# Optimization experiments

Measured on AMD Instinct MI355X. Metric: run time of the kernel, lower is better.

Reference implementation:

```python
import jax, jax.numpy as jnp
import numpy as np

# dims: M scalars (0e), K vectors (1e) in input; T = tp_features; N = batch of atoms
M, K, T, N = 128, 64, 64, 131072
D_IN = M + 3 * K  # 320, e3nn layout: [128x0e | 64x1e flattened as (mul, 3)]


def _act_norm(f):
    # e3nn Activation normalizes act so E_{z~N(0,1)}[act(z)^2] = 1
    z = np.linspace(-8.0, 8.0, 20001)
    pdf = np.exp(-0.5 * z * z) / np.sqrt(2.0 * np.pi)
    return float(np.sqrt(np.trapz(f(z) ** 2 * pdf, z)))

C_SILU = _act_norm(lambda z: z / (1.0 + np.exp(-z)))
C_RELU = _act_norm(lambda z: np.maximum(z, 0.0))
INV_SQRT_M = float(1.0 / np.sqrt(M))
INV_SQRT_K = float(1.0 / np.sqrt(K))
INV_SQRT_3 = float(1.0 / np.sqrt(3.0))  # wigner_3j(1,1,0) = delta_ij/sqrt(3)
TP_NORM = float(1.0 / np.sqrt(2.0 * T * T))  # fan-in over the 2 paths into 0e


def setup_inputs() -> dict:
    key = jax.random.key(0)
    ks = jax.random.split(key, 11)
    f32 = jnp.float32
    return {
        "x": jax.random.normal(ks[0], (N, D_IN), f32),
        "input_shift": jnp.zeros((D_IN,), f32),
        "output_scale": jnp.ones((), f32),
        # PerceptronLayer 1: Linear (Mx0e+Kx1e) -> ((M+K)x0e + Kx1e)
        "w0_1": jax.random.normal(ks[1], (M, M + K), f32),
        "b0_1": jnp.zeros((M + K,), f32),
        "w1_1": jax.random.normal(ks[2], (K, K), f32),
        # PerceptronLayer 2 (same irreps, resnet applies)
        "w0_2": jax.random.normal(ks[3], (M, M + K), f32),
        "b0_2": jnp.zeros((M + K,), f32),
        "w1_2": jax.random.normal(ks[4], (K, K), f32),
        # linear_out: (Mx0e+Kx1e) -> (Tx0e+Tx1e)
        "w0_o": jax.random.normal(ks[5], (M, T), f32),
        "b0_o": jnp.zeros((T,), f32),
        "w1_o": jax.random.normal(ks[6], (K, T), f32),
        # FullyConnectedTensorProduct (tp, tp) -> 1x0e: paths 0e*0e->0e, 1e*1e->0e
        "w_tp0": jax.random.normal(ks[7], (T, T), f32),
        "w_tp1": jax.random.normal(ks[8], (T, T), f32),
    }


def _linear(xs, xv, w0, b0, w1):
    # e3nn o3.Linear: per-irrep dense mixing with 1/sqrt(fan_in), bias on 0e only
    ys = xs @ w0 * INV_SQRT_M + b0          # [N, M+K] scalars + gates
    yv = jnp.einsum('nki,kj->nji', xv, w1) * INV_SQRT_K  # [N, K, 3]
    return ys, yv


def _gate(ys, yv):
    # e3nn Gate: silu on 0e scalars, relu on 0e gates, gate the 1e vectors
    s = jax.nn.silu(ys[:, :M]) / C_SILU     # [N, M]
    g = jax.nn.relu(ys[:, M:]) / C_RELU     # [N, K]
    return s, yv * g[:, :, None]


def reference(x, input_shift, output_scale,
              w0_1, b0_1, w1_1, w0_2, b0_2, w1_2,
              w0_o, b0_o, w1_o, w_tp0, w_tp1):
    x = x - input_shift
    xs = x[:, :M]                           # [N, M] 0e block
    xv = x[:, M:].reshape(-1, K, 3)         # [N, K, 3] 1e block
    for (w0, b0, w1) in ((w0_1, b0_1, w1_1), (w0_2, b0_2, w1_2)):
        ys, yv = _linear(xs, xv, w0, b0, w1)
        s, v = _gate(ys, yv)
        xs = xs + s                         # resnet: irreps_in == irreps_out
        xv = xv + v
    # linear_out -> irreps_tp = Tx0e + Tx1e
    zs = xs @ w0_o * INV_SQRT_M + b0_o                    # [N, T]
    zv = jnp.einsum('nki,kj->nji', xv, w1_o) * INV_SQRT_K # [N, T, 3]
    # FullyConnectedTensorProduct(z, z) -> 0e (avoid [N,T,T] blowup)
    y0 = jnp.sum((zs @ w_tp0) * zs, axis=-1)                                    # [N]
    y1 = jnp.sum(jnp.einsum('nui,uv->nvi', zv, w_tp1) * zv, axis=(1, 2)) * INV_SQRT_3
    y = (y0 + y1) * TP_NORM / output_scale
    return y[:, None]
```

## Files before the change

kernel.cpp:

```cpp
#include <hip/hip_runtime.h>
#include <math.h>


typedef _Float16 f16;
typedef _Float16 f16x8 __attribute__((ext_vector_type(8)));
typedef __fp16   fp16x2 __attribute__((ext_vector_type(2)));
typedef float    f32x4 __attribute__((ext_vector_type(4)));
typedef int      i32x4 __attribute__((ext_vector_type(4)));

#define MFMA16(a, b, c) __builtin_amdgcn_mfma_f32_16x16x32_f16(a, b, c, 0, 0, 0)

constexpr float INV_SQRT_M = 0.08838834764831845f;
constexpr float INV_SQRT_K = 0.125f;
constexpr float INV_SQRT_3 = 0.57735026918962576f;
constexpr float TP_NORM    = 0.011048543456039806f;

#define OFF_W01 0
#define OFF_W11 24576
#define OFF_W02 28672
#define OFF_W12 53248
#define OFF_W0O 57344
#define OFF_W1O 65536
#define OFF_TP0 69632
#define OFF_TP1 73728
#define PACK_UNITS 9728
#define FB01 38912
#define FB02 39104
#define FB0O 39296
#define TOTAL_UNITS (PACK_UNITS + 448)

#define LDS_W1     24576
#define LDS_BIAS_F 14336
#define LDS_W0O    0
#define LDS_W1O    8192
#define LDS_TP0    12288
#define LDS_TP1    16384
#define LDS_B0O_F  10240

#define NTHR 512

__global__ void pack_and_consts(const float* __restrict__ w01, const float* __restrict__ w11,
                                const float* __restrict__ w02, const float* __restrict__ w12,
                                const float* __restrict__ w0o, const float* __restrict__ w1o,
                                const float* __restrict__ tp0, const float* __restrict__ tp1,
                                const float* __restrict__ b01, const float* __restrict__ b02,
                                const float* __restrict__ b0o,
                                f16* __restrict__ dst, float* __restrict__ ws) {
    if (blockIdx.x == 40) {
        __shared__ double red[256];
        const int t = threadIdx.x;
        double acc_s = 0.0, acc_r = 0.0;
        for (int i = t; i <= 20000; i += 256) {
            const double z = -8.0 + (16.0 * (double)i) / 20000.0;
            const double pdf = exp(-0.5 * z * z) / 2.5066282746310002;
            const double sil = z / (1.0 + exp(-z));
            const double wgt = (i == 0 || i == 20000) ? 0.5 : 1.0;
            acc_s += wgt * sil * sil * pdf;
            if (z > 0.0) acc_r += wgt * z * z * pdf;
        }
        red[t] = acc_s;
        __syncthreads();
        for (int o = 128; o > 0; o >>= 1) { if (t < o) red[t] += red[t + o]; __syncthreads(); }
        const double tot_s = red[0];
        __syncthreads();
        red[t] = acc_r;
        __syncthreads();
        for (int o = 128; o > 0; o >>= 1) { if (t < o) red[t] += red[t + o]; __syncthreads(); }
        if (t == 0) {
            const double dz = 16.0 / 20000.0;
            ws[0] = (float)(1.0 / sqrt(tot_s * dz));
            ws[1] = (float)(1.0 / sqrt(red[0] * dz));
        }
        return;
    }
    int u = blockIdx.x * 256 + threadIdx.x;
    if (u >= TOTAL_UNITS) return;
    if (u >= PACK_UNITS) {
        const int idx = u - PACK_UNITS;
        float* dstF = (float*)dst;
        if (idx < 192)      dstF[FB01 + idx] = b01[idx];
        else if (idx < 384) dstF[FB02 + (idx - 192)] = b02[idx - 192];
        else                dstF[FB0O + (idx - 384)] = b0o[idx - 384];
        return;
    }
    const float* src; int NC, base, lu = u; float sc;
    if      (lu < 3072) {            src = w01; NC = 192; base = OFF_W01; sc = INV_SQRT_M; }
    else if (lu < 3584) { lu -= 3072; src = w11; NC = 64;  base = OFF_W11; sc = INV_SQRT_K; }
    else if (lu < 6656) { lu -= 3584; src = w02; NC = 192; base = OFF_W02; sc = INV_SQRT_M; }
    else if (lu < 7168) { lu -= 6656; src = w12; NC = 64;  base = OFF_W12; sc = INV_SQRT_K; }
    else if (lu < 8192) { lu -= 7168; src = w0o; NC = 64;  base = OFF_W0O; sc = INV_SQRT_M; }
    else if (lu < 8704) { lu -= 8192; src = w1o; NC = 64;  base = OFF_W1O; sc = INV_SQRT_K; }
    else if (lu < 9216) { lu -= 8704; src = tp0; NC = 64;  base = OFF_TP0; sc = 1.0f; }
    else                { lu -= 9216; src = tp1; NC = 64;  base = OFF_TP1; sc = INV_SQRT_3; }
    const int lane = lu & 63;
    const int frag = lu >> 6;
    const int NT = NC >> 4;
    const int kstep = frag / NT, nj = frag - kstep * NT;
    const int gl  = lane >> 4;
    const int col = nj * 16 + (lane & 15);
    f16 tmp[8];
    #pragma unroll
    for (int e = 0; e < 8; ++e) {
        const int row = kstep * 32 + ((e >> 2) << 4) + (gl << 2) + (e & 3);
        tmp[e] = (f16)(src[(size_t)row * NC + col] * sc);
    }
    *(f16x8*)&dst[(size_t)(base) + (size_t)lu * 8] = *(f16x8*)tmp;
}

__device__ __forceinline__ int pk2i(float a, float b) {
    union { fp16x2 h; int i; } u;
    u.h = __builtin_amdgcn_cvt_pkrtz(a, b);
    return u.i;
}

__device__ __forceinline__ f16x8 packB(f32x4 t0, f32x4 t1) {
    union { i32x4 i; f16x8 v; } u;
    u.i[0] = pk2i(t0[0], t0[1]);
    u.i[1] = pk2i(t0[2], t0[3]);
    u.i[2] = pk2i(t1[0], t1[1]);
    u.i[3] = pk2i(t1[2], t1[3]);
    return u.v;
}

union Frag { f16x8 v; fp16x2 h2[4]; };

__device__ __forceinline__ void resblock32(
    Frag (&xsS)[2][4], Frag (&xvS)[2][3][2],
    const f16* lds, float invCS, float invCR, int l, int g)
{
    const float* biasF = (const float*)lds + LDS_BIAS_F;

    f16x8 xsB[2][4];
    #pragma unroll
    for (int h = 0; h < 2; ++h)
        #pragma unroll
        for (int ks = 0; ks < 4; ++ks)
            xsB[h][ks] = xsS[h][ks].v;

    float gate[2][4][4];
    #pragma unroll
    for (int nj = 0; nj < 12; ++nj) {
        f32x4 acc0 = {0.f, 0.f, 0.f, 0.f}, acc1 = {0.f, 0.f, 0.f, 0.f};
        #pragma unroll
        for (int ks = 0; ks < 4; ++ks) {
            const f16x8 a = *(const f16x8*)&lds[(size_t)((ks * 12 + nj) * 64 + l) * 8];
            acc0 = MFMA16(a, xsB[0][ks], acc0);
            acc1 = MFMA16(a, xsB[1][ks], acc1);
        }
        const f32x4 bias = *(const f32x4*)&biasF[nj * 16 + g * 4];
        #pragma unroll
        for (int h = 0; h < 2; ++h) {
            const f32x4 acc = h ? acc1 : acc0;
            if (nj < 8) {
                float s[4];
                #pragma unroll
                for (int r = 0; r < 4; ++r) {
                    const float ys = acc[r] + bias[r];
                    s[r] = ys * __builtin_amdgcn_rcpf(1.0f + __expf(-ys)) * invCS;
                }
                xsS[h][nj >> 1].h2[2 * (nj & 1)]     += __builtin_amdgcn_cvt_pkrtz(s[0], s[1]);
                xsS[h][nj >> 1].h2[2 * (nj & 1) + 1] += __builtin_amdgcn_cvt_pkrtz(s[2], s[3]);
            } else {
                #pragma unroll
                for (int r = 0; r < 4; ++r) {
                    const float ys = acc[r] + bias[r];
                    gate[h][nj - 8][r] = fmaxf(ys, 0.f) * invCR;
                }
            }
        }
    }

    f16x8 xvB[2][3][2];
    #pragma unroll
    for (int h = 0; h < 2; ++h)
        #pragma unroll
        for (int i = 0; i < 3; ++i)
            #pragma unroll
            for (int ks = 0; ks < 2; ++ks)
                xvB[h][i][ks] = xvS[h][i][ks].v;

    #pragma unroll
    for (int i = 0; i < 3; ++i)
        #pragma unroll
        for (int nj = 0; nj < 4; ++nj) {
            f32x4 acc0 = {0.f, 0.f, 0.f, 0.f}, acc1 = {0.f, 0.f, 0.f, 0.f};
            #pragma unroll
            for (int ks = 0; ks < 2; ++ks) {
                const f16x8 a = *(const f16x8*)&lds[LDS_W1 + (size_t)((ks * 4 + nj) * 64 + l) * 8];
                acc0 = MFMA16(a, xvB[0][i][ks], acc0);
                acc1 = MFMA16(a, xvB[1][i][ks], acc1);
            }
            #pragma unroll
            for (int h = 0; h < 2; ++h) {
                const f32x4 acc = h ? acc1 : acc0;
                float u[4];
                #pragma unroll
                for (int r = 0; r < 4; ++r)
                    u[r] = acc[r] * gate[h][nj][r];
                xvS[h][i][nj >> 1].h2[2 * (nj & 1)]     += __builtin_amdgcn_cvt_pkrtz(u[0], u[1]);
                xvS[h][i][nj >> 1].h2[2 * (nj & 1) + 1] += __builtin_amdgcn_cvt_pkrtz(u[2], u[3]);
            }
        }
}

__global__ __launch_bounds__(NTHR, 2)
void corrnet_lds(const float* __restrict__ x, const float* __restrict__ shift,
                 const float* __restrict__ oscale,
                 const f16* __restrict__ wp, const float* __restrict__ consts,
                 float* __restrict__ out)
{
    __shared__ __align__(16) f16 smem[29056];
    float* smemF = (float*)smem;
    const float* wpF = (const float*)wp;

    const int t = threadIdx.x;
    const int l = t & 63;
    const int g = l >> 4;
    const int c = l & 15;
    const size_t n0 = (size_t)blockIdx.x * 256 + (size_t)(t >> 6) * 32;

    const float invCS = consts[0], invCR = consts[1];
    const float inv_os = 1.0f / oscale[0];

    Frag xsS[2][4];
    Frag xvS[2][3][2];
    #pragma unroll
    for (int h = 0; h < 2; ++h) {
        const float* xrow = x + (n0 + h * 16 + c) * 320;
        #pragma unroll
        for (int ks = 0; ks < 4; ++ks) {
            const int col = ks * 32 + g * 4;
            const f32x4 t0 = *(const f32x4*)(xrow + col)      - *(const f32x4*)(shift + col);
            const f32x4 t1 = *(const f32x4*)(xrow + col + 16) - *(const f32x4*)(shift + col + 16);
            xsS[h][ks].v = packB(t0, t1);
        }
        f32x4 tmp[3][4];
        #pragma unroll
        for (int tau = 0; tau < 4; ++tau) {
            const int col = 128 + 3 * (tau * 16 + g * 4);
            const f32x4 a0 = *(const f32x4*)(xrow + col)     - *(const f32x4*)(shift + col);
            const f32x4 a1 = *(const f32x4*)(xrow + col + 4) - *(const f32x4*)(shift + col + 4);
            const f32x4 a2 = *(const f32x4*)(xrow + col + 8) - *(const f32x4*)(shift + col + 8);
            float arr[12];
            #pragma unroll
            for (int e = 0; e < 4; ++e) {
                arr[e] = a0[e]; arr[4 + e] = a1[e]; arr[8 + e] = a2[e];
            }
            #pragma unroll
            for (int r = 0; r < 4; ++r)
                #pragma unroll
                for (int i = 0; i < 3; ++i)
                    tmp[i][tau][r] = arr[3 * r + i];
        }
        #pragma unroll
        for (int i = 0; i < 3; ++i)
            #pragma unroll
            for (int ks = 0; ks < 2; ++ks)
                xvS[h][i][ks].v = packB(tmp[i][2 * ks], tmp[i][2 * ks + 1]);
    }

    #pragma clang loop unroll(disable)
    for (int b = 0; b < 2; ++b) {
        const size_t woff = b ? (size_t)OFF_W02 : (size_t)OFF_W01;
        const size_t boff = b ? (size_t)FB02    : (size_t)FB01;
        #pragma unroll
        for (int it = 0; it < 7; ++it) {
            const int u = it * NTHR + t;
            *(f16x8*)&smem[(size_t)u * 8] = *(const f16x8*)&wp[woff + (size_t)u * 8];
        }
        if (t < 48)
            ((f32x4*)&smemF[LDS_BIAS_F])[t] = ((const f32x4*)&wpF[boff])[t];
        __syncthreads();
        resblock32(xsS, xvS, smem, invCS, invCR, l, g);
        __syncthreads();
    }

    #pragma unroll
    for (int it = 0; it < 5; ++it) {
        const int u = it * NTHR + t;
        *(f16x8*)&smem[(size_t)u * 8] = *(const f16x8*)&wp[(size_t)(OFF_W0O) + (size_t)u * 8];
    }
    if (t < 16)
        ((f32x4*)&smemF[LDS_B0O_F])[t] = ((const f32x4*)&wpF[FB0O])[t];
    __syncthreads();

    f32x4 zs[2][4];
    #pragma unroll
    for (int nj = 0; nj < 4; ++nj) {
        f32x4 acc0 = {0.f, 0.f, 0.f, 0.f}, acc1 = {0.f, 0.f, 0.f, 0.f};
        #pragma unroll
        for (int ks = 0; ks < 4; ++ks) {
            const f16x8 a = *(const f16x8*)&smem[LDS_W0O + (size_t)((ks * 4 + nj) * 64 + l) * 8];
            acc0 = MFMA16(a, xsS[0][ks].v, acc0);
            acc1 = MFMA16(a, xsS[1][ks].v, acc1);
        }
        const f32x4 bias = *(const f32x4*)&smemF[LDS_B0O_F + nj * 16 + g * 4];
        #pragma unroll
        for (int r = 0; r < 4; ++r) {
            zs[0][nj][r] = acc0[r] + bias[r];
            zs[1][nj][r] = acc1[r] + bias[r];
        }
    }

    float part[2]  = {0.f, 0.f};
    float part1[2] = {0.f, 0.f};

    {
        f16x8 zsB[2][2];
        #pragma unroll
        for (int h = 0; h < 2; ++h)
            #pragma unroll
            for (int ks = 0; ks < 2; ++ks)
                zsB[h][ks] = packB(zs[h][2 * ks], zs[h][2 * ks + 1]);
        #pragma unroll
        for (int nj = 0; nj < 4; ++nj) {
            f32x4 acc0 = {0.f, 0.f, 0.f, 0.f}, acc1 = {0.f, 0.f, 0.f, 0.f};
            #pragma unroll
            for (int ks = 0; ks < 2; ++ks) {
                const f16x8 a = *(const f16x8*)&smem[LDS_TP0 + (size_t)((ks * 4 + nj) * 64 + l) * 8];
                acc0 = MFMA16(a, zsB[0][ks], acc0);
                acc1 = MFMA16(a, zsB[1][ks], acc1);
            }
            #pragma unroll
            for (int r = 0; r < 4; ++r) {
                part[0] += acc0[r] * zs[0][nj][r];
                part[1] += acc1[r] * zs[1][nj][r];
            }
        }
    }

    #pragma unroll
    for (int i = 0; i < 3; ++i) {
        f32x4 zv[2][4];
        #pragma unroll
        for (int nj = 0; nj < 4; ++nj) {
            f32x4 acc0 = {0.f, 0.f, 0.f, 0.f}, acc1 = {0.f, 0.f, 0.f, 0.f};
            #pragma unroll
            for (int ks = 0; ks < 2; ++ks) {
                const f16x8 a = *(const f16x8*)&smem[LDS_W1O + (size_t)((ks * 4 + nj) * 64 + l) * 8];
                acc0 = MFMA16(a, xvS[0][i][ks].v, acc0);
                acc1 = MFMA16(a, xvS[1][i][ks].v, acc1);
            }
            #pragma unroll
            for (int r = 0; r < 4; ++r) {
                zv[0][nj][r] = acc0[r];
                zv[1][nj][r] = acc1[r];
            }
        }
        f16x8 zvB[2][2];
        #pragma unroll
        for (int h = 0; h < 2; ++h)
            #pragma unroll
            for (int ks = 0; ks < 2; ++ks)
                zvB[h][ks] = packB(zv[h][2 * ks], zv[h][2 * ks + 1]);
        #pragma unroll
        for (int nj = 0; nj < 4; ++nj) {
            f32x4 acc0 = {0.f, 0.f, 0.f, 0.f}, acc1 = {0.f, 0.f, 0.f, 0.f};
            #pragma unroll
            for (int ks = 0; ks < 2; ++ks) {
                const f16x8 a = *(const f16x8*)&smem[LDS_TP1 + (size_t)((ks * 4 + nj) * 64 + l) * 8];
                acc0 = MFMA16(a, zvB[0][ks], acc0);
                acc1 = MFMA16(a, zvB[1][ks], acc1);
            }
            #pragma unroll
            for (int r = 0; r < 4; ++r) {
                part1[0] += acc0[r] * zv[0][nj][r];
                part1[1] += acc1[r] * zv[1][nj][r];
            }
        }
    }
    #pragma unroll
    for (int h = 0; h < 2; ++h)
        part[h] += part1[h];

    #pragma unroll
    for (int h = 0; h < 2; ++h) {
        part[h] += __shfl_xor(part[h], 16, 64);
        part[h] += __shfl_xor(part[h], 32, 64);
    }

    if (l < 16)
        out[n0 + l] = part[0] * TP_NORM * inv_os;
    else if (l < 32)
        out[n0 + 16 + (l - 16)] = part[1] * TP_NORM * inv_os;
}

extern "C" void kernel_launch(void* const* d_in, const int* in_sizes, int n_in,
                              void* d_out, int out_size, void* d_ws, size_t ws_size,
                              hipStream_t stream) {
    const float* x      = (const float*)d_in[0];
    const float* shift  = (const float*)d_in[1];
    const float* oscale = (const float*)d_in[2];
    const float* w01    = (const float*)d_in[3];
    const float* b01    = (const float*)d_in[4];
    const float* w11    = (const float*)d_in[5];
    const float* w02    = (const float*)d_in[6];
    const float* b02    = (const float*)d_in[7];
    const float* w12    = (const float*)d_in[8];
    const float* w0o    = (const float*)d_in[9];
    const float* b0o    = (const float*)d_in[10];
    const float* w1o    = (const float*)d_in[11];
    const float* wtp0   = (const float*)d_in[12];
    const float* wtp1   = (const float*)d_in[13];
    float* out    = (float*)d_out;
    float* consts = (float*)d_ws;
    f16*   wp     = (f16*)((char*)d_ws + 16);

    pack_and_consts<<<41, 256, 0, stream>>>(
        w01, w11, w02, w12, w0o, w1o, wtp0, wtp1, b01, b02, b0o, wp, consts);

    const int nblocks = 131072 / 256;
    corrnet_lds<<<nblocks, NTHR, 0, stream>>>(
        x, shift, oscale, wp, consts, out);
}
```

Before: 79.32 us.

## Stage input rows through LDS with coalesced loads and permute row-to-wave mapping

Input x is now loaded cooperatively in 32-row chunks with fully coalesced float4 reads into a padded LDS buffer (stride 332), then each wave picks its MFMA fragments out of LDS. Previously each lane read strided 16-byte pieces directly from global memory. The row-to-wave assignment is permuted so that each wave owns rows interleaved across the chunks, and the output indexing is changed to match. The resblock loop is also manually unrolled. The cost is 16 extra barriers and LDS traffic in exchange for better global coalescing.

Result: no change. 80.32 us (+1.3%).

```diff
diff --git a/kernel.cpp b/kernel.cpp
--- a/kernel.cpp
+++ b/kernel.cpp
@@ -38,6 +38,7 @@
 #define LDS_B0O_F  10240
 
 #define NTHR 512
+#define XSTR 332
 
 __global__ void pack_and_consts(const float* __restrict__ w01, const float* __restrict__ w11,
                                 const float* __restrict__ w02, const float* __restrict__ w12,
@@ -215,9 +216,10 @@
 
     const int t = threadIdx.x;
     const int l = t & 63;
+    const int w = __builtin_amdgcn_readfirstlane(t >> 6);
     const int g = l >> 4;
     const int c = l & 15;
-    const size_t n0 = (size_t)blockIdx.x * 256 + (size_t)(t >> 6) * 32;
+    const size_t nblk = (size_t)blockIdx.x * 256;
 
     const float invCS = consts[0], invCR = consts[1];
     const float inv_os = 1.0f / oscale[0];
@@ -225,55 +227,77 @@
     Frag xsS[2][4];
     Frag xvS[2][3][2];
     #pragma unroll
-    for (int h = 0; h < 2; ++h) {
-        const float* xrow = x + (n0 + h * 16 + c) * 320;
-        #pragma unroll
-        for (int ks = 0; ks < 4; ++ks) {
-            const int col = ks * 32 + g * 4;
-            const f32x4 t0 = *(const f32x4*)(xrow + col)      - *(const f32x4*)(shift + col);
-            const f32x4 t1 = *(const f32x4*)(xrow + col + 16) - *(const f32x4*)(shift + col + 16);
-            xsS[h][ks].v = packB(t0, t1);
-        }
-        f32x4 tmp[3][4];
-        #pragma unroll
-        for (int tau = 0; tau < 4; ++tau) {
-            const int col = 128 + 3 * (tau * 16 + g * 4);
-            const f32x4 a0 = *(const f32x4*)(xrow + col)     - *(const f32x4*)(shift + col);
-            const f32x4 a1 = *(const f32x4*)(xrow + col + 4) - *(const f32x4*)(shift + col + 4);
-            const f32x4 a2 = *(const f32x4*)(xrow + col + 8) - *(const f32x4*)(shift + col + 8);
-            float arr[12];
-            #pragma unroll
-            for (int e = 0; e < 4; ++e) {
-                arr[e] = a0[e]; arr[4 + e] = a1[e]; arr[8 + e] = a2[e];
-            }
-            #pragma unroll
-            for (int r = 0; r < 4; ++r)
-                #pragma unroll
-                for (int i = 0; i < 3; ++i)
-                    tmp[i][tau][r] = arr[3 * r + i];
-        }
-        #pragma unroll
-        for (int i = 0; i < 3; ++i)
-            #pragma unroll
-            for (int ks = 0; ks < 2; ++ks)
-                xvS[h][i][ks].v = packB(tmp[i][2 * ks], tmp[i][2 * ks + 1]);
-    }
-
-    #pragma clang loop unroll(disable)
-    for (int b = 0; b < 2; ++b) {
-        const size_t woff = b ? (size_t)OFF_W02 : (size_t)OFF_W01;
-        const size_t boff = b ? (size_t)FB02    : (size_t)FB01;
-        #pragma unroll
-        for (int it = 0; it < 7; ++it) {
-            const int u = it * NTHR + t;
-            *(f16x8*)&smem[(size_t)u * 8] = *(const f16x8*)&wp[woff + (size_t)u * 8];
-        }
-        if (t < 48)
-            ((f32x4*)&smemF[LDS_BIAS_F])[t] = ((const f32x4*)&wpF[boff])[t];
+    for (int p = 0; p < 8; ++p) {
+        const float* xbase = x + (nblk + (size_t)p * 32) * 320;
+        #pragma unroll
+        for (int it = 0; it < 5; ++it) {
+            const int q  = it * NTHR + t;
+            const int r  = q / 80;
+            const int c4 = (q - r * 80) * 4;
+            const f32x4 v = *(const f32x4*)(xbase + (size_t)r * 320 + c4)
+                          - *(const f32x4*)(shift + c4);
+            *(f32x4*)&smemF[r * XSTR + c4] = v;
+        }
         __syncthreads();
-        resblock32(xsS, xvS, smem, invCS, invCR, l, g);
+        const int h  = p >> 2;
+        const int cb = (p & 3) << 2;
+        if ((c & 12) == cb) {
+            const float* rowp = smemF + (w * 4 + (c & 3)) * XSTR;
+            #pragma unroll
+            for (int ks = 0; ks < 4; ++ks) {
+                const int col = ks * 32 + g * 4;
+                const f32x4 t0 = *(const f32x4*)(rowp + col);
+                const f32x4 t1 = *(const f32x4*)(rowp + col + 16);
+                xsS[h][ks].v = packB(t0, t1);
+            }
+            f32x4 tmp[3][4];
+            #pragma unroll
+            for (int tau = 0; tau < 4; ++tau) {
+                const int col = 128 + 3 * (tau * 16 + g * 4);
+                const f32x4 a0 = *(const f32x4*)(rowp + col);
+                const f32x4 a1 = *(const f32x4*)(rowp + col + 4);
+                const f32x4 a2 = *(const f32x4*)(rowp + col + 8);
+                float arr[12];
+                #pragma unroll
+                for (int e = 0; e < 4; ++e) {
+                    arr[e] = a0[e]; arr[4 + e] = a1[e]; arr[8 + e] = a2[e];
+                }
+                #pragma unroll
+                for (int r = 0; r < 4; ++r)
+                    #pragma unroll
+                    for (int i = 0; i < 3; ++i)
+                        tmp[i][tau][r] = arr[3 * r + i];
+            }
+            #pragma unroll
+            for (int i = 0; i < 3; ++i)
+                #pragma unroll
+                for (int ks = 0; ks < 2; ++ks)
+                    xvS[h][i][ks].v = packB(tmp[i][2 * ks], tmp[i][2 * ks + 1]);
+        }
         __syncthreads();
     }
+
+    #pragma unroll
+    for (int it = 0; it < 7; ++it) {
+        const int u = it * NTHR + t;
+        *(f16x8*)&smem[(size_t)u * 8] = *(const f16x8*)&wp[(size_t)u * 8];
+    }
+    if (t < 48)
+        ((f32x4*)&smemF[LDS_BIAS_F])[t] = ((const f32x4*)&wpF[FB01])[t];
+    __syncthreads();
+    resblock32(xsS, xvS, smem, invCS, invCR, l, g);
+    __syncthreads();
+
+    #pragma unroll
+    for (int it = 0; it < 7; ++it) {
+        const int u = it * NTHR + t;
+        *(f16x8*)&smem[(size_t)u * 8] = *(const f16x8*)&wp[(size_t)(OFF_W02) + (size_t)u * 8];
+    }
+    if (t < 48)
+        ((f32x4*)&smemF[LDS_BIAS_F])[t] = ((const f32x4*)&wpF[FB02])[t];
+    __syncthreads();
+    resblock32(xsS, xvS, smem, invCS, invCR, l, g);
+    __syncthreads();
 
     #pragma unroll
     for (int it = 0; it < 5; ++it) {
@@ -380,9 +404,11 @@
     }
 
     if (l < 16)
-        out[n0 + l] = part[0] * TP_NORM * inv_os;
-    else if (l < 32)
-        out[n0 + 16 + (l - 16)] = part[1] * TP_NORM * inv_os;
+        out[nblk + (size_t)((l >> 2) * 32) + w * 4 + (l & 3)] = part[0] * TP_NORM * inv_os;
+    else if (l < 32) {
+        const int cc = l - 16;
+        out[nblk + (size_t)((4 + (cc >> 2)) * 32) + w * 4 + (cc & 3)] = part[1] * TP_NORM * inv_os;
+    }
 }
 
 extern "C" void kernel_launch(void* const* d_in, const int* in_sizes, int n_in,
```
